# Performance work log

Measured on AMD Instinct MI355X. Metric: run time of the kernel, lower is better.

The kernel has to match this reference:

```python
import jax, jax.numpy as jnp
import numpy as np

NEG_SLOPE = 0.01  # torch F.leaky_relu default
EPS = 1e-12


def setup_inputs() -> dict:
    key = jax.random.key(0)
    k1, k2, k3, k4 = jax.random.split(key, 4)
    num_nodes, in_f, out_f, num_edges = 50000, 128, 128, 600000
    x = jax.random.normal(k1, (num_nodes, in_f), dtype=jnp.float32)
    edge_index = jax.random.randint(k2, (2, num_edges), 0, num_nodes, dtype=jnp.int64)
    # xavier_uniform for W:[out,in]
    limit = float(np.sqrt(6.0 / (in_f + out_f)))
    W = jax.random.uniform(k3, (out_f, in_f), dtype=jnp.float32, minval=-limit, maxval=limit)
    a = jax.random.uniform(k4, (2 * out_f,), dtype=jnp.float32, minval=0.0, maxval=1.0)
    return {"x": x, "edge_index": edge_index, "W": W, "a": a}


def reference(x, edge_index, W, a):
    num_nodes = x.shape[0]
    out_f = W.shape[0]
    # add self loops
    loops = jnp.arange(num_nodes, dtype=edge_index.dtype)
    src = jnp.concatenate([edge_index[0], loops])
    dst = jnp.concatenate([edge_index[1], loops])
    messages = x @ W.T                      # [N, F_out]
    # cat([h_src,h_dst]) @ a == h_src @ a[:F] + h_dst @ a[F:] (avoids materializing concat)
    s_src = messages @ a[:out_f]            # [N]
    s_dst = messages @ a[out_f:]            # [N]
    e_ij = jax.nn.leaky_relu(s_src[src] + s_dst[dst], negative_slope=NEG_SLOPE)  # [E]
    w = jnp.exp(e_ij)                       # unnormalized edge weights
    denom = jax.ops.segment_sum(w, dst, num_segments=num_nodes)
    denom = jnp.maximum(denom, EPS)
    weighted = w[:, None] * messages[src]   # [E, F_out]
    agg = jax.ops.segment_sum(weighted, dst, num_segments=num_nodes)
    return agg / denom[:, None]
```

## Files before the change

kernel.cpp:

```cpp
#include <hip/hip_runtime.h>

#define NEG_SLOPE 0.01f
#define CAP 64

typedef __attribute__((ext_vector_type(8))) short bf16x8;
typedef __attribute__((ext_vector_type(4))) float f32x4;

static __device__ __forceinline__ unsigned short f2bf(float f) {
  unsigned u = __float_as_uint(f);
  u += 0x7fffu + ((u >> 16) & 1u);
  return (unsigned short)(u >> 16);
}

__global__ __launch_bounds__(256) void k_setup(const float* __restrict__ W,
                                               const float* __restrict__ a,
                                               unsigned short* __restrict__ Wb,
                                               float* __restrict__ p_lo,
                                               float* __restrict__ p_hi,
                                               int* __restrict__ counts, int N, int nz) {
  int b = blockIdx.x;
  int t = threadIdx.x;
  if (b < nz) {
    int i = b * 256 + t;
    if (i < N) counts[i] = 0;
  } else if (b < nz + 64) {
    int i = (b - nz) * 256 + t;
    Wb[i] = f2bf(W[i]);
  } else {
    if (t < 128) {
      float lo = 0.f, hi = 0.f;
#pragma unroll 8
      for (int f = 0; f < 128; ++f) {
        float w = W[f * 128 + t];
        lo += w * a[f];
        hi += w * a[128 + f];
      }
      p_lo[t] = lo;
      p_hi[t] = hi;
    }
  }
}

__global__ __launch_bounds__(256) void k_work(const float* __restrict__ x,
                                              const float* __restrict__ p_lo,
                                              const float* __restrict__ p_hi,
                                              const unsigned short* __restrict__ Wb,
                                              unsigned short* __restrict__ msgs,
                                              float* __restrict__ s_src,
                                              float* __restrict__ s_dst, int N,
                                              const int* __restrict__ ei,
                                              int* __restrict__ counts,
                                              unsigned* __restrict__ edges, int E,
                                              int SB) {
  if ((int)blockIdx.x < SB) {
    int e2 = blockIdx.x * 256 + threadIdx.x;
    int e = e2 * 2;
    if (e >= E) return;
    int2 srcp = *(const int2*)(ei + e);
    int2 dstp = *(const int2*)(ei + E + e);
    int pos0 = atomicAdd(&counts[dstp.x], 1);
    if (pos0 < CAP) edges[(size_t)dstp.x * CAP + pos0] = (unsigned)srcp.x;
    if (e + 1 < E) {
      int pos1 = atomicAdd(&counts[dstp.y], 1);
      if (pos1 < CAP) edges[(size_t)dstp.y * CAP + pos1] = (unsigned)srcp.y;
    }
    return;
  }
  int bb = blockIdx.x - SB;
  int wave = (bb * 256 + (int)threadIdx.x) >> 6;
  int lane = threadIdx.x & 63;
  int base = wave * 16;
  if (base >= N) return;
  int q = lane >> 4, r = lane & 15;
  int node = base + r;
  const float* xrow = x + (size_t)node * 128 + q * 8;
  const float4* pl = (const float4*)p_lo;
  const float4* ph = (const float4*)p_hi;
  bf16x8 afrag[4];
  float lo = 0.f, hi = 0.f;
#pragma unroll
  for (int c = 0; c < 4; ++c) {
    float4 v0 = *(const float4*)(xrow + c * 32);
    float4 v1 = *(const float4*)(xrow + c * 32 + 4);
    int fi = q * 2 + c * 8;
    float4 a0 = pl[fi], a1 = pl[fi + 1];
    float4 b0 = ph[fi], b1 = ph[fi + 1];
    lo += v0.x * a0.x + v0.y * a0.y + v0.z * a0.z + v0.w * a0.w
        + v1.x * a1.x + v1.y * a1.y + v1.z * a1.z + v1.w * a1.w;
    hi += v0.x * b0.x + v0.y * b0.y + v0.z * b0.z + v0.w * b0.w
        + v1.x * b1.x + v1.y * b1.y + v1.z * b1.z + v1.w * b1.w;
    bf16x8 f;
    f[0] = (short)f2bf(v0.x); f[1] = (short)f2bf(v0.y);
    f[2] = (short)f2bf(v0.z); f[3] = (short)f2bf(v0.w);
    f[4] = (short)f2bf(v1.x); f[5] = (short)f2bf(v1.y);
    f[6] = (short)f2bf(v1.z); f[7] = (short)f2bf(v1.w);
    afrag[c] = f;
  }
  lo += __shfl_xor(lo, 16); lo += __shfl_xor(lo, 32);
  hi += __shfl_xor(hi, 16); hi += __shfl_xor(hi, 32);
  if (q == 0) { s_src[node] = lo; s_dst[node] = hi; }
#pragma unroll
  for (int ft = 0; ft < 8; ++ft) {
    const unsigned short* wrow = Wb + (size_t)(ft * 16 + r) * 128 + q * 8;
    f32x4 acc = {0.f, 0.f, 0.f, 0.f};
#pragma unroll
    for (int c = 0; c < 4; ++c) {
      bf16x8 bfrag = *(const bf16x8*)(wrow + c * 32);
      acc = __builtin_amdgcn_mfma_f32_16x16x32_bf16(afrag[c], bfrag, acc, 0, 0, 0);
    }
#pragma unroll
    for (int rr = 0; rr < 4; ++rr) {
      int n2 = base + q * 4 + rr;
      msgs[(size_t)n2 * 128 + ft * 16 + r] = f2bf(acc[rr]);
    }
  }
}

__global__ __launch_bounds__(256) void k_agg(const unsigned short* __restrict__ msgs,
                                             const int* __restrict__ counts,
                                             const unsigned* __restrict__ edges,
                                             const float* __restrict__ s_src,
                                             const float* __restrict__ s_dst,
                                             float* __restrict__ out, int N) {
  int wave = (blockIdx.x * 256 + threadIdx.x) >> 6;
  int lane = threadIdx.x & 63;
  if (wave >= N) return;
  int node = wave;
  int g = lane >> 4;
  int r = lane & 15;
  float sdn = s_dst[node];
  float zs = s_src[node] + sdn;
  zs = zs > 0.f ? zs : NEG_SLOPE * zs;
  float wself = expf(zs);
  float wg = (g == 0) ? wself : 0.f;
  float denom = wg;
  float acc[8];
  {
    const uint4* mrow = (const uint4*)(msgs + (size_t)node * 128);
    uint4 m = mrow[r];
    unsigned mm[4] = {m.x, m.y, m.z, m.w};
#pragma unroll
    for (int c = 0; c < 4; ++c) {
      acc[2 * c]     = wg * __uint_as_float(mm[c] << 16);
      acc[2 * c + 1] = wg * __uint_as_float(mm[c] & 0xffff0000u);
    }
  }
  int cnt = counts[node];
  cnt = cnt < CAP ? cnt : CAP;
  const unsigned* bucket = edges + (size_t)node * CAP;
  int nIter = (cnt + 15) >> 4;
  for (int it = 0; it < nIter; ++it) {
    int kb = it * 16 + g;
    bool v[4];
    unsigned e[4];
    uint4 m[4];
    float ss[4];
#pragma unroll
    for (int u = 0; u < 4; ++u) {
      int k = kb + u * 4;
      v[u] = k < cnt;
      e[u] = bucket[v[u] ? k : 0];
    }
#pragma unroll
    for (int u = 0; u < 4; ++u)
      m[u] = ((const uint4*)(msgs + (size_t)e[u] * 128))[r];
#pragma unroll
    for (int u = 0; u < 4; ++u)
      ss[u] = s_src[e[u]];
#pragma unroll
    for (int u = 0; u < 4; ++u) {
      float z = ss[u] + sdn;
      z = z > 0.f ? z : NEG_SLOPE * z;
      float w = v[u] ? expf(z) : 0.f;
      unsigned mm[4] = {m[u].x, m[u].y, m[u].z, m[u].w};
#pragma unroll
      for (int c = 0; c < 4; ++c) {
        acc[2 * c]     += w * __uint_as_float(mm[c] << 16);
        acc[2 * c + 1] += w * __uint_as_float(mm[c] & 0xffff0000u);
      }
      denom += w;
    }
  }
#pragma unroll
  for (int mask = 16; mask < 64; mask <<= 1) {
#pragma unroll
    for (int j = 0; j < 8; ++j) acc[j] += __shfl_xor(acc[j], mask);
    denom += __shfl_xor(denom, mask);
  }
  if (g == 0) {
    float inv = 1.f / fmaxf(denom, 1e-12f);
    float4 o0 = {acc[0] * inv, acc[1] * inv, acc[2] * inv, acc[3] * inv};
    float4 o1 = {acc[4] * inv, acc[5] * inv, acc[6] * inv, acc[7] * inv};
    float4* orow = (float4*)(out + (size_t)node * 128);
    orow[r * 2] = o0;
    orow[r * 2 + 1] = o1;
  }
}

extern "C" void kernel_launch(void* const* d_in, const int* in_sizes, int n_in,
                              void* d_out, int out_size, void* d_ws, size_t ws_size,
                              hipStream_t stream) {
  const float* x = (const float*)d_in[0];
  const int* ei = (const int*)d_in[1];
  const float* W = (const float*)d_in[2];
  const float* a = (const float*)d_in[3];
  float* out = (float*)d_out;
  int N = in_sizes[0] / 128;
  int E = in_sizes[1] / 2;

  char* ws = (char*)d_ws;
  size_t off = 0;
  auto alloc = [&](size_t bytes) {
    off = (off + 255) & ~(size_t)255;
    void* p = ws + off;
    off += bytes;
    return p;
  };
  unsigned short* msgs = (unsigned short*)alloc((size_t)N * 128 * 2);
  float* s_src = (float*)alloc((size_t)N * 4);
  float* s_dst = (float*)alloc((size_t)N * 4);
  float* p_lo = (float*)alloc(512);
  float* p_hi = (float*)alloc(512);
  unsigned short* Wb = (unsigned short*)alloc(128 * 128 * 2);
  int* counts = (int*)alloc((size_t)N * 4);
  unsigned* edges = (unsigned*)alloc((size_t)N * CAP * 4);

  int nz = (N + 255) / 256;
  int waves = (N + 15) / 16;
  int SB = ((E + 1) / 2 + 255) / 256;
  int MB = (waves + 3) / 4;
  k_setup<<<nz + 64 + 1, 256, 0, stream>>>(W, a, Wb, p_lo, p_hi, counts, N, nz);
  k_work<<<SB + MB, 256, 0, stream>>>(x, p_lo, p_hi, Wb, msgs, s_src, s_dst, N,
                                      ei, counts, edges, E, SB);
  k_agg<<<(N + 3) / 4, 256, 0, stream>>>(msgs, counts, edges, s_src, s_dst, out, N);
}
```

Measured before the change: 159.5 us.

## Replace per-node atomic bucket fill with two-pass binned CSR construction

Edge bucketing moves from global per-destination atomics into fixed-capacity buckets to a two-pass scheme. First, blocks histogram edges into coarse 512-node bins in shared memory and scatter them into per-bin buffers. Then a second kernel builds a compact CSR with per-node offsets and counts for the aggregation kernel. This cuts global atomic traffic and scattered writes and removes the per-node cap, at the cost of an extra kernel launch, larger k_work shared memory (32KB staging), and a fixed bin capacity that could overflow on skewed inputs.

```diff
diff --git a/kernel.cpp b/kernel.cpp
--- a/kernel.cpp
+++ b/kernel.cpp
@@ -1,7 +1,10 @@
 #include <hip/hip_runtime.h>
 
 #define NEG_SLOPE 0.01f
-#define CAP 64
+#define CH 4096
+#define BSHIFT 9
+#define BINW 512
+#define NBMAX 128
 
 typedef __attribute__((ext_vector_type(8))) short bf16x8;
 typedef __attribute__((ext_vector_type(4))) float f32x4;
@@ -17,15 +20,13 @@
                                                unsigned short* __restrict__ Wb,
                                                float* __restrict__ p_lo,
                                                float* __restrict__ p_hi,
-                                               int* __restrict__ counts, int N, int nz) {
+                                               int* __restrict__ bin_cursor) {
   int b = blockIdx.x;
   int t = threadIdx.x;
-  if (b < nz) {
+  if (b < 64) {
     int i = b * 256 + t;
-    if (i < N) counts[i] = 0;
-  } else if (b < nz + 64) {
-    int i = (b - nz) * 256 + t;
     Wb[i] = f2bf(W[i]);
+    if (b == 0 && t < NBMAX) bin_cursor[t] = 0;
   } else {
     if (t < 128) {
       float lo = 0.f, hi = 0.f;
@@ -49,30 +50,66 @@
                                               float* __restrict__ s_src,
                                               float* __restrict__ s_dst, int N,
                                               const int* __restrict__ ei,
-                                              int* __restrict__ counts,
-                                              unsigned* __restrict__ edges, int E,
-                                              int SB) {
+                                              int* __restrict__ bin_cursor,
+                                              int2* __restrict__ binbuf, int E,
+                                              int SB, int BINCAP) {
+  __shared__ int hist[NBMAX], base[NBMAX], cur[NBMAX], gbase[NBMAX];
+  __shared__ int2 stage[CH];
+  int t = threadIdx.x;
   if ((int)blockIdx.x < SB) {
-    int e2 = blockIdx.x * 256 + threadIdx.x;
-    int e = e2 * 2;
-    if (e >= E) return;
-    int2 srcp = *(const int2*)(ei + e);
-    int2 dstp = *(const int2*)(ei + E + e);
-    int pos0 = atomicAdd(&counts[dstp.x], 1);
-    if (pos0 < CAP) edges[(size_t)dstp.x * CAP + pos0] = (unsigned)srcp.x;
-    if (e + 1 < E) {
-      int pos1 = atomicAdd(&counts[dstp.y], 1);
-      if (pos1 < CAP) edges[(size_t)dstp.y * CAP + pos1] = (unsigned)srcp.y;
+    int e0 = blockIdx.x * CH;
+    int cntE = E - e0; if (cntE > CH) cntE = CH;
+    if (t < NBMAX) { hist[t] = 0; cur[t] = 0; }
+    __syncthreads();
+    int srcs[CH / 256], dsts[CH / 256];
+#pragma unroll
+    for (int j = 0; j < CH / 256; ++j) {
+      int i = t + j * 256;
+      if (i < cntE) {
+        srcs[j] = ei[e0 + i];
+        dsts[j] = ei[E + e0 + i];
+        atomicAdd(&hist[dsts[j] >> BSHIFT], 1);
+      }
+    }
+    __syncthreads();
+    if (t < NBMAX) base[t] = hist[t];
+    __syncthreads();
+    for (int d = 1; d < NBMAX; d <<= 1) {
+      int v = (t < NBMAX && t >= d) ? base[t - d] : 0;
+      __syncthreads();
+      if (t < NBMAX) base[t] += v;
+      __syncthreads();
+    }
+    if (t < NBMAX) {
+      base[t] -= hist[t];
+      gbase[t] = hist[t] ? atomicAdd(&bin_cursor[t], hist[t]) : 0;
+    }
+    __syncthreads();
+#pragma unroll
+    for (int j = 0; j < CH / 256; ++j) {
+      int i = t + j * 256;
+      if (i < cntE) {
+        int bin = dsts[j] >> BSHIFT;
+        int p = base[bin] + atomicAdd(&cur[bin], 1);
+        stage[p] = make_int2(srcs[j], dsts[j]);
+      }
+    }
+    __syncthreads();
+    for (int i = t; i < cntE; i += 256) {
+      int2 ed = stage[i];
+      int bin = ed.y >> BSHIFT;
+      int idx = gbase[bin] + (i - base[bin]);
+      if (idx < BINCAP) binbuf[(size_t)bin * BINCAP + idx] = ed;
     }
     return;
   }
   int bb = blockIdx.x - SB;
-  int wave = (bb * 256 + (int)threadIdx.x) >> 6;
-  int lane = threadIdx.x & 63;
-  int base = wave * 16;
-  if (base >= N) return;
+  int wave = (bb * 256 + t) >> 6;
+  int lane = t & 63;
+  int baseN = wave * 16;
+  if (baseN >= N) return;
   int q = lane >> 4, r = lane & 15;
-  int node = base + r;
+  int node = baseN + r;
   const float* xrow = x + (size_t)node * 128 + q * 8;
   const float4* pl = (const float4*)p_lo;
   const float4* ph = (const float4*)p_hi;
@@ -110,15 +147,58 @@
     }
 #pragma unroll
     for (int rr = 0; rr < 4; ++rr) {
-      int n2 = base + q * 4 + rr;
+      int n2 = baseN + q * 4 + rr;
       msgs[(size_t)n2 * 128 + ft * 16 + r] = f2bf(acc[rr]);
     }
   }
 }
 
+__global__ __launch_bounds__(256) void k_pass2(const int2* __restrict__ binbuf,
+                                               const int* __restrict__ bin_cursor,
+                                               unsigned* __restrict__ csr,
+                                               int2* __restrict__ meta,
+                                               int N, int BINCAP) {
+  __shared__ int hist[BINW], scanv[BINW], cur[BINW];
+  __shared__ int tmp[256];
+  int b = blockIdx.x, t = threadIdx.x;
+  int cnt = bin_cursor[b]; if (cnt > BINCAP) cnt = BINCAP;
+  const int2* bb = binbuf + (size_t)b * BINCAP;
+  hist[t] = 0; hist[t + 256] = 0;
+  __syncthreads();
+  for (int i = t; i < cnt; i += 256)
+    atomicAdd(&hist[bb[i].y & (BINW - 1)], 1);
+  __syncthreads();
+  int v0 = hist[2 * t], v1 = hist[2 * t + 1];
+  tmp[t] = v0 + v1;
+  __syncthreads();
+  for (int d = 1; d < 256; d <<= 1) {
+    int v = (t >= d) ? tmp[t - d] : 0;
+    __syncthreads();
+    tmp[t] += v;
+    __syncthreads();
+  }
+  int excl = tmp[t] - (v0 + v1);
+  scanv[2 * t] = excl;
+  scanv[2 * t + 1] = excl + v0;
+  cur[2 * t] = 0; cur[2 * t + 1] = 0;
+  __syncthreads();
+  int gb = b * BINCAP;
+  for (int l = t; l < BINW; l += 256) {
+    int dst = b * BINW + l;
+    if (dst < N) meta[dst] = make_int2(gb + scanv[l], hist[l]);
+  }
+  __syncthreads();
+  for (int i = t; i < cnt; i += 256) {
+    int2 ed = bb[i];
+    int l = ed.y & (BINW - 1);
+    int p = atomicAdd(&cur[l], 1);
+    csr[gb + scanv[l] + p] = (unsigned)ed.x;
+  }
+}
+
 __global__ __launch_bounds__(256) void k_agg(const unsigned short* __restrict__ msgs,
-                                             const int* __restrict__ counts,
-                                             const unsigned* __restrict__ edges,
+                                             const int2* __restrict__ meta,
+                                             const unsigned* __restrict__ csr,
                                              const float* __restrict__ s_src,
                                              const float* __restrict__ s_dst,
                                              float* __restrict__ out, int N) {
@@ -145,9 +225,9 @@
       acc[2 * c + 1] = wg * __uint_as_float(mm[c] & 0xffff0000u);
     }
   }
-  int cnt = counts[node];
-  cnt = cnt < CAP ? cnt : CAP;
-  const unsigned* bucket = edges + (size_t)node * CAP;
+  int2 md = meta[node];
+  int cnt = md.y;
+  const unsigned* bucket = csr + md.x;
   int nIter = (cnt + 15) >> 4;
   for (int it = 0; it < nIter; ++it) {
     int kb = it * 16 + g;
@@ -207,6 +287,9 @@
   float* out = (float*)d_out;
   int N = in_sizes[0] / 128;
   int E = in_sizes[1] / 2;
+
+  int NB = (N + BINW - 1) >> BSHIFT;
+  int BINCAP = ((E / NB) + (E / NB) / 4 + 1024 + 255) & ~255;
 
   char* ws = (char*)d_ws;
   size_t off = 0;
@@ -222,15 +305,17 @@
   float* p_lo = (float*)alloc(512);
   float* p_hi = (float*)alloc(512);
   unsigned short* Wb = (unsigned short*)alloc(128 * 128 * 2);
-  int* counts = (int*)alloc((size_t)N * 4);
-  unsigned* edges = (unsigned*)alloc((size_t)N * CAP * 4);
-
-  int nz = (N + 255) / 256;
+  int* bin_cursor = (int*)alloc(NBMAX * 4);
+  int2* binbuf = (int2*)alloc((size_t)NB * BINCAP * 8);
+  unsigned* csr = (unsigned*)alloc((size_t)NB * BINCAP * 4);
+  int2* meta = (int2*)alloc((size_t)N * 8);
+
   int waves = (N + 15) / 16;
-  int SB = ((E + 1) / 2 + 255) / 256;
+  int SB = (E + CH - 1) / CH;
   int MB = (waves + 3) / 4;
-  k_setup<<<nz + 64 + 1, 256, 0, stream>>>(W, a, Wb, p_lo, p_hi, counts, N, nz);
+  k_setup<<<65, 256, 0, stream>>>(W, a, Wb, p_lo, p_hi, bin_cursor);
   k_work<<<SB + MB, 256, 0, stream>>>(x, p_lo, p_hi, Wb, msgs, s_src, s_dst, N,
-                                      ei, counts, edges, E, SB);
-  k_agg<<<(N + 3) / 4, 256, 0, stream>>>(msgs, counts, edges, s_src, s_dst, out, N);
-}
+                                      ei, bin_cursor, binbuf, E, SB, BINCAP);
+  k_pass2<<<NB, 256, 0, stream>>>(binbuf, bin_cursor, csr, meta, N, BINCAP);
+  k_agg<<<(N + 3) / 4, 256, 0, stream>>>(msgs, meta, csr, s_src, s_dst, out, N);
+}
```

Result: faster. 147.8 us (-7.4%).
